# Optimization experiments

Measured on AMD Instinct MI355X. Metric: run time of the kernel, lower is better.

Reference implementation:

```python
import jax, jax.numpy as jnp
import numpy as np

GRID = 8
SPACING = 2.0
RADIUS = 3.0
B = 64
CODE = 1024
HID = 128
L = 4
EPS = 1e-5


def _layernorm(h, g, b):
    mu = h.mean(-1, keepdims=True)
    var = ((h - mu) ** 2).mean(-1, keepdims=True)
    return (h - mu) * jax.lax.rsqrt(var + EPS) * g + b


def setup_inputs() -> dict:
    key = jax.random.key(0)
    ks = jax.random.split(key, 16)
    n = GRID ** 3
    # grid coords, centered, spacing=anchor_spacing (create_grid_coords)
    idx = np.arange(GRID)
    coords = (np.stack(np.meshgrid(idx, idx, idx, indexing='ij'), -1).reshape(-1, 3)
              - (GRID - 1) / 2.0) * SPACING
    # radius_graph per batch: identical geometry per graph -> offset base edges
    d2 = ((coords[:, None, :] - coords[None, :, :]) ** 2).sum(-1)
    mask = (d2 <= RADIUS ** 2) & (d2 > 0)
    r0, c0 = np.nonzero(mask)
    off = (np.arange(B) * n)[:, None]
    row = (r0[None, :] + off).reshape(-1)
    col = (c0[None, :] + off).reshape(-1)
    edge_index = jnp.asarray(np.stack([row, col]), dtype=jnp.int32)  # [2,E]
    grid_coords = jnp.asarray(np.tile(coords, (B, 1)), dtype=jnp.float32)  # [B*n,3]
    s = 0.02
    inp = {
        'y': jax.random.normal(ks[0], (B, n, CODE), jnp.float32),
        'grid_coords': grid_coords,
        'edge_index': edge_index,
        'W_in': jax.random.normal(ks[1], (HID, CODE), jnp.float32) * s,
        'b_in': jnp.zeros((HID,), jnp.float32),
        'gam': jnp.ones((L, HID), jnp.float32),
        'bet': jnp.zeros((L, HID), jnp.float32),
        'eW1': jax.random.normal(ks[2], (L, HID, 2 * HID + 1), jnp.float32) * s,
        'eb1': jnp.zeros((L, HID), jnp.float32),
        'eW2': jax.random.normal(ks[3], (L, HID, HID), jnp.float32) * s,
        'eb2': jnp.zeros((L, HID), jnp.float32),
        'nW1': jax.random.normal(ks[4], (L, HID, 2 * HID), jnp.float32) * s,
        'nb1': jnp.zeros((L, HID), jnp.float32),
        'nW2': jax.random.normal(ks[5], (L, HID, HID), jnp.float32) * s,
        'nb2': jnp.zeros((L, HID), jnp.float32),
        'W_out': jax.random.normal(ks[6], (CODE, HID), jnp.float32) * s,
        'b_out': jnp.zeros((CODE,), jnp.float32),
    }
    return inp


def reference(y, grid_coords, edge_index, W_in, b_in, gam, bet,
              eW1, eb1, eW2, eb2, nW1, nb1, nW2, nb2, W_out, b_out):
    N = grid_coords.shape[0]  # B*n nodes
    row, col = edge_index[0], edge_index[1]
    rel = grid_coords[col] - grid_coords[row]            # [E,3]
    dist = jnp.linalg.norm(rel, axis=-1, keepdims=True)  # [E,1]
    cnt = jax.ops.segment_sum(jnp.ones((row.shape[0],), y.dtype), col, num_segments=N)
    inv_cnt = jnp.where(cnt > 0, 1.0 / jnp.maximum(cnt, 1.0), 0.0)[:, None]  # [N,1]

    h = jnp.einsum('bnc,hc->bnh', y, W_in) + b_in
    h = h.reshape(N, HID)
    for l in range(L):
        hn = _layernorm(h, gam[l], bet[l])               # [N,H]
        e_in = jnp.concatenate([hn[row], hn[col], dist], axis=-1)  # [E,2H+1]
        m = jax.nn.silu(e_in @ eW1[l].T + eb1[l])
        m = jax.nn.silu(m @ eW2[l].T + eb2[l])           # [E,H]
        m_aggr = jax.ops.segment_sum(m, col, num_segments=N) * inv_cnt  # scatter-mean
        d = jax.nn.silu(jnp.concatenate([hn, m_aggr], axis=-1) @ nW1[l].T + nb1[l])
        d = d @ nW2[l].T + nb2[l]
        h = hn + d                                        # residual on normalized h
    h = h.reshape(B, -1, HID)
    return jnp.einsum('bnh,ch->bnc', h, W_out) + b_out
```

## Files before the change

kernel.cpp:

```cpp
#include <hip/hip_runtime.h>
#include <math.h>


#define HIDDEN 128
#define NLAYERS 4
#define NBASE 512
#define NB 64
#define CODE 1024

typedef __attribute__((ext_vector_type(8))) short s16x8;
typedef __attribute__((ext_vector_type(4))) float f32x4;

__device__ __forceinline__ unsigned int cvt_pk_bf16(float lo, float hi) {
    unsigned int d;
    asm("v_cvt_pk_bf16_f32 %0, %1, %2" : "=v"(d) : "v"(lo), "v"(hi));
    return d;
}
__device__ __forceinline__ unsigned short f2bf(float x) {
    return (unsigned short)cvt_pk_bf16(x, x);
}
__device__ __forceinline__ float bf2f(unsigned short b) {
    return __uint_as_float(((unsigned int)b) << 16);
}
__device__ __forceinline__ float silu_f(float x) {
    float e = __expf(-x);
    float r;
    asm("v_rcp_f32 %0, %1" : "=v"(r) : "v"(1.f + e));
    return x * r;
}
__device__ __forceinline__ void light_barrier() {
    __builtin_amdgcn_sched_barrier(0);
    asm volatile("s_waitcnt lgkmcnt(0)" ::: "memory");
    __builtin_amdgcn_s_barrier();
    __builtin_amdgcn_sched_barrier(0);
}

__device__ __forceinline__ void conv_body(
    const float* __restrict__ s, unsigned short* __restrict__ d,
    int blk, int tid, int n) {
    int i = (blk * 256 + tid) * 4;
    if (i >= n) return;
    float4 v = *reinterpret_cast<const float4*>(s + i);
    uint2 o = { cvt_pk_bf16(v.x, v.y), cvt_pk_bf16(v.z, v.w) };
    *reinterpret_cast<uint2*>(d + i) = o;
}

__global__ __launch_bounds__(256) void prep_all(
    const float* __restrict__ W_in, const float* __restrict__ W_out,
    const float* __restrict__ nW1, const float* __restrict__ nW2,
    const float* __restrict__ eW2, const float* __restrict__ eW1,
    const float* __restrict__ eb1,
    const int* __restrict__ row, const int* __restrict__ col,
    const float* __restrict__ gc,
    unsigned short* __restrict__ winbf, unsigned short* __restrict__ woutbf,
    unsigned short* __restrict__ wn1bf, unsigned short* __restrict__ wn2bf,
    unsigned short* __restrict__ w2bf, unsigned short* __restrict__ w1ab,
    float* __restrict__ c01,
    int* __restrict__ brp, int* __restrict__ bcol, int baseE) {
    int blk = blockIdx.x, tid = threadIdx.x;
    if (blk < 128)      { conv_body(W_in,  winbf,  blk,       tid, HIDDEN * CODE); return; }
    if (blk < 256)      { conv_body(W_out, woutbf, blk - 128, tid, CODE * HIDDEN); return; }
    if (blk < 384)      { conv_body(nW1,   wn1bf,  blk - 256, tid, NLAYERS * HIDDEN * 256); return; }
    if (blk < 448)      { conv_body(nW2,   wn2bf,  blk - 384, tid, NLAYERS * HIDDEN * HIDDEN); return; }
    if (blk < 512)      { conv_body(eW2,   w2bf,   blk - 448, tid, NLAYERS * HIDDEN * HIDDEN); return; }
    if (blk < 516) {
        int l = blk - 512;
        const float* w = eW1 + (size_t)l * HIDDEN * 257;
        for (int i = tid; i < 256 * 128; i += 256) {
            int n = i >> 7, k = i & 127;
            float v = (n < 128) ? w[(size_t)n * 257 + k]
                                : w[(size_t)(n - 128) * 257 + 128 + k];
            w1ab[(size_t)l * 256 * 128 + i] = f2bf(v);
        }
        if (tid < 128) {
            float wd = w[(size_t)tid * 257 + 256];
            c01[(size_t)l * 256 + tid] = 2.f * wd;
            c01[(size_t)l * 256 + 128 + tid] = sqrtf(8.f) * wd;
        }
        return;
    }
    if (blk < 519) {
        int v = (blk - 516) * 256 + tid;
        if (v > NBASE) return;
        int lo = 0, hi = baseE;
        while (lo < hi) {
            int mid = (lo + hi) >> 1;
            if (row[mid] < v) lo = mid + 1; else hi = mid;
        }
        brp[v] = lo;
        return;
    }
    {
        int t = (blk - 519) * 256 + tid;
        if (t >= baseE) return;
        int u = col[t], v = row[t];
        float dx = gc[(size_t)u * 3 + 0] - gc[(size_t)v * 3 + 0];
        float dy = gc[(size_t)u * 3 + 1] - gc[(size_t)v * 3 + 1];
        float dz = gc[(size_t)u * 3 + 2] - gc[(size_t)v * 3 + 2];
        float d2 = dx * dx + dy * dy + dz * dz;
        bcol[t] = u | ((d2 > 6.f ? 1 : 0) << 15);
    }
}

__global__ __launch_bounds__(256) void mgemm64(
    const unsigned short* __restrict__ A, int K,
    const unsigned short* __restrict__ W,
    const float* __restrict__ bias,
    float* __restrict__ Cf, unsigned short* __restrict__ Cb, int ldC, int perm) {
    __shared__ __align__(16) unsigned short As[64 * 128];
    __shared__ __align__(16) unsigned short Ws[128 * 128];
    int tid = threadIdx.x;
    int wid = tid >> 6, l = tid & 63, lr = l & 15, lg = l >> 4;
    int wm = wid >> 1, wn = wid & 1;
    int row0 = blockIdx.x * 64;
    int cb = blockIdx.y * 128;
    f32x4 acc[2][4];
#pragma unroll
    for (int i = 0; i < 2; ++i)
#pragma unroll
        for (int j = 0; j < 4; ++j) {
            f32x4 z = { 0.f, 0.f, 0.f, 0.f };
            acc[i][j] = z;
        }
    for (int kc = 0; kc < K; kc += 128) {
#pragma unroll
        for (int jj = 0; jj < 4; ++jj) {
            int j = tid + jj * 256;
            int r = j >> 4, c = j & 15;
            int srow = row0 + r;
            if (perm == 3) srow = ((srow & 511) << 6) | (srow >> 9);
            s16x8 v = *reinterpret_cast<const s16x8*>(
                A + (size_t)srow * K + kc + c * 8);
            *reinterpret_cast<s16x8*>(&As[r * 128 + ((c ^ (r & 7)) << 3)]) = v;
        }
#pragma unroll
        for (int jj = 0; jj < 8; ++jj) {
            int j = tid + jj * 256;
            int r = j >> 4, c = j & 15;
            s16x8 wv = *reinterpret_cast<const s16x8*>(
                W + (size_t)(cb + r) * K + kc + c * 8);
            *reinterpret_cast<s16x8*>(&Ws[r * 128 + ((c ^ (r & 7)) << 3)]) = wv;
        }
        light_barrier();
#pragma unroll
        for (int ks = 0; ks < 4; ++ks) {
            int c = ks * 4 + lg;
            s16x8 af[2], bf[4];
#pragma unroll
            for (int mi = 0; mi < 2; ++mi) {
                int r = wm * 32 + mi * 16 + lr;
                af[mi] = *reinterpret_cast<s16x8*>(&As[r * 128 + ((c ^ (r & 7)) << 3)]);
            }
#pragma unroll
            for (int ni = 0; ni < 4; ++ni) {
                int n = wn * 64 + ni * 16 + lr;
                bf[ni] = *reinterpret_cast<s16x8*>(&Ws[n * 128 + ((c ^ (n & 7)) << 3)]);
            }
#pragma unroll
            for (int mi = 0; mi < 2; ++mi)
#pragma unroll
                for (int ni = 0; ni < 4; ++ni)
                    acc[mi][ni] = __builtin_amdgcn_mfma_f32_16x16x32_bf16(
                        af[mi], bf[ni], acc[mi][ni], 0, 0, 0);
        }
        light_barrier();
    }
#pragma unroll
    for (int mi = 0; mi < 2; ++mi) {
#pragma unroll
        for (int ni = 0; ni < 4; ++ni) {
            int colg = cb + wn * 64 + ni * 16 + lr;
            float bs = bias ? bias[colg] : 0.f;
#pragma unroll
            for (int r4 = 0; r4 < 4; ++r4) {
                int rowg = row0 + wm * 32 + mi * 16 + lg * 4 + r4;
                float v = acc[mi][ni][r4] + bs;
                if (Cf) Cf[(size_t)rowg * ldC + colg] = v;
                if (Cb) Cb[(size_t)rowg * ldC + colg] = f2bf(v);
            }
        }
    }
}

__global__ __launch_bounds__(256) void inproj_ln(
    const float* __restrict__ y,
    const unsigned short* __restrict__ W, const float* __restrict__ bias,
    const float* __restrict__ g, const float* __restrict__ bet,
    unsigned short* __restrict__ hnbf,
    const unsigned short* __restrict__ w1ab0,
    const float* __restrict__ eb1_0,
    unsigned short* __restrict__ ab_out) {
    __shared__ __align__(16) unsigned short As[64 * 128];
    __shared__ __align__(16) unsigned short Ws[128 * 128];
    int tid = threadIdx.x;
    int wid = tid >> 6, l = tid & 63, lr = l & 15, lg = l >> 4;
    int row0 = blockIdx.x * 64;
    f32x4 acc[8];
#pragma unroll
    for (int ni = 0; ni < 8; ++ni) {
        f32x4 z = { 0.f, 0.f, 0.f, 0.f };
        acc[ni] = z;
    }
    float4 pa0[4], pa1[4];
    s16x8 pw[8];
    auto loadc = [&](int kc) {
#pragma unroll
        for (int jj = 0; jj < 4; ++jj) {
            int j = tid + jj * 256, r = j >> 4, c = j & 15;
            const float* p = y + (size_t)(row0 + r) * CODE + kc + c * 8;
            pa0[jj] = *reinterpret_cast<const float4*>(p);
            pa1[jj] = *reinterpret_cast<const float4*>(p + 4);
        }
#pragma unroll
        for (int jj = 0; jj < 8; ++jj) {
            int j = tid + jj * 256, r = j >> 4, c = j & 15;
            pw[jj] = *reinterpret_cast<const s16x8*>(W + (size_t)r * CODE + kc + c * 8);
        }
    };
    auto storec = [&]() {
#pragma unroll
        for (int jj = 0; jj < 4; ++jj) {
            int j = tid + jj * 256, r = j >> 4, c = j & 15;
            union { s16x8 s; unsigned int w[4]; } pk;
            pk.w[0] = cvt_pk_bf16(pa0[jj].x, pa0[jj].y);
            pk.w[1] = cvt_pk_bf16(pa0[jj].z, pa0[jj].w);
            pk.w[2] = cvt_pk_bf16(pa1[jj].x, pa1[jj].y);
            pk.w[3] = cvt_pk_bf16(pa1[jj].z, pa1[jj].w);
            *reinterpret_cast<s16x8*>(&As[r * 128 + ((c ^ (r & 7)) << 3)]) = pk.s;
        }
#pragma unroll
        for (int jj = 0; jj < 8; ++jj) {
            int j = tid + jj * 256, r = j >> 4, c = j & 15;
            *reinterpret_cast<s16x8*>(&Ws[r * 128 + ((c ^ (r & 7)) << 3)]) = pw[jj];
        }
    };
    loadc(0);
    for (int kc8 = 0; kc8 < 8; ++kc8) {
        storec();
        light_barrier();
        if (kc8 < 7) loadc((kc8 + 1) * 128);
#pragma unroll
        for (int ks = 0; ks < 4; ++ks) {
            int c = ks * 4 + lg;
            int r = wid * 16 + lr;
            s16x8 af = *reinterpret_cast<s16x8*>(&As[r * 128 + ((c ^ (r & 7)) << 3)]);
#pragma unroll
            for (int ni = 0; ni < 8; ++ni) {
                int n = ni * 16 + lr;
                s16x8 bf = *reinterpret_cast<s16x8*>(&Ws[n * 128 + ((c ^ (n & 7)) << 3)]);
                acc[ni] = __builtin_amdgcn_mfma_f32_16x16x32_bf16(af, bf, acc[ni], 0, 0, 0);
            }
        }
        light_barrier();
    }
#pragma unroll
    for (int ni = 0; ni < 8; ++ni) {
        float bs = bias[ni * 16 + lr];
#pragma unroll
        for (int r4 = 0; r4 < 4; ++r4) acc[ni][r4] += bs;
    }
    float s[4], q[4];
#pragma unroll
    for (int r4 = 0; r4 < 4; ++r4) {
        float ss = 0.f, qq = 0.f;
#pragma unroll
        for (int ni = 0; ni < 8; ++ni) {
            float v = acc[ni][r4];
            ss += v; qq += v * v;
        }
#pragma unroll
        for (int o = 1; o < 16; o <<= 1) {
            ss += __shfl_xor(ss, o, 64);
            qq += __shfl_xor(qq, o, 64);
        }
        float mu = ss * (1.f / 128.f);
        float var = qq * (1.f / 128.f) - mu * mu;
        s[r4] = mu;
        q[r4] = rsqrtf(var + 1e-5f);
    }
#pragma unroll
    for (int ni = 0; ni < 8; ++ni) {
        int col = ni * 16 + lr;
        float gg = g[col], bb = bet[col];
        int cc = col >> 3, cin = col & 7;
#pragma unroll
        for (int r4 = 0; r4 < 4; ++r4) {
            int rowg = row0 + wid * 16 + lg * 4 + r4;
            int orow = (rowg & 511) * 64 + (rowg >> 9);
            float o = (acc[ni][r4] - s[r4]) * q[r4] * gg + bb;
            hnbf[(size_t)orow * HIDDEN + col] = f2bf(o);
            int rl = wid * 16 + lg * 4 + r4;
            As[rl * 128 + ((cc ^ (rl & 7)) << 3) + cin] = f2bf(o);
        }
    }
#pragma unroll
    for (int half = 0; half < 2; ++half) {
#pragma unroll
        for (int jj = 0; jj < 8; ++jj) {
            int j = tid + jj * 256;
            int r = j >> 4, c = j & 15;
            s16x8 wv = *reinterpret_cast<const s16x8*>(
                w1ab0 + (size_t)(half * 128 + r) * 128 + c * 8);
            *reinterpret_cast<s16x8*>(&Ws[r * 128 + ((c ^ (r & 7)) << 3)]) = wv;
        }
        light_barrier();
#pragma unroll
        for (int ni = 0; ni < 8; ++ni) {
            f32x4 z = { 0.f, 0.f, 0.f, 0.f };
            acc[ni] = z;
        }
#pragma unroll
        for (int ks = 0; ks < 4; ++ks) {
            int c = ks * 4 + lg;
            int r = wid * 16 + lr;
            s16x8 af = *reinterpret_cast<s16x8*>(&As[r * 128 + ((c ^ (r & 7)) << 3)]);
#pragma unroll
            for (int ni = 0; ni < 8; ++ni) {
                int n = ni * 16 + lr;
                s16x8 bf = *reinterpret_cast<s16x8*>(&Ws[n * 128 + ((c ^ (n & 7)) << 3)]);
                acc[ni] = __builtin_amdgcn_mfma_f32_16x16x32_bf16(af, bf, acc[ni], 0, 0, 0);
            }
        }
#pragma unroll
        for (int ni = 0; ni < 8; ++ni) {
            int col = ni * 16 + lr;
            float bs = half ? eb1_0[col] : 0.f;
#pragma unroll
            for (int r4 = 0; r4 < 4; ++r4) {
                int rowg = row0 + wid * 16 + lg * 4 + r4;
                int orow = (rowg & 511) * 64 + (rowg >> 9);
                ab_out[(size_t)orow * 256 + half * 128 + col] =
                    f2bf(acc[ni][r4] + bs);
            }
        }
        if (half == 0) light_barrier();
    }
}

__global__ __launch_bounds__(256) void nmlp_ln(
    unsigned short* __restrict__ hnbf,
    const unsigned short* __restrict__ magbf,
    const unsigned short* __restrict__ w1, const float* __restrict__ b1,
    const unsigned short* __restrict__ w2, const float* __restrict__ b2,
    const float* __restrict__ g, const float* __restrict__ bet,
    unsigned short* __restrict__ hbf_out,
    const unsigned short* __restrict__ w1ab_next,
    const float* __restrict__ eb1_next,
    unsigned short* __restrict__ ab_out) {
    __shared__ __align__(16) unsigned short As[64 * 128];
    __shared__ __align__(16) unsigned short Ws[128 * 128];
    int tid = threadIdx.x;
    int wid = tid >> 6, l = tid & 63, lr = l & 15, lg = l >> 4;
    int row0 = blockIdx.x * 64;
    int myrow = row0 + wid * 16 + lr;
    f32x4 acc[8];
#pragma unroll
    for (int ni = 0; ni < 8; ++ni) {
        f32x4 z = { 0.f, 0.f, 0.f, 0.f };
        acc[ni] = z;
    }
    for (int kc = 0; kc < 2; ++kc) {
        const unsigned short* Xsrc = kc ? magbf : hnbf;
#pragma unroll
        for (int jj = 0; jj < 8; ++jj) {
            int j = tid + jj * 256;
            int r = j >> 4, c = j & 15;
            s16x8 wv = *reinterpret_cast<const s16x8*>(
                w1 + (size_t)r * 256 + kc * 128 + c * 8);
            *reinterpret_cast<s16x8*>(&Ws[r * 128 + ((c ^ (r & 7)) << 3)]) = wv;
        }
        light_barrier();
#pragma unroll
        for (int ks = 0; ks < 4; ++ks) {
            s16x8 af = *reinterpret_cast<const s16x8*>(
                Xsrc + (size_t)myrow * 128 + ks * 32 + lg * 8);
#pragma unroll
            for (int ni = 0; ni < 8; ++ni) {
                int n = ni * 16 + lr;
                int c = ks * 4 + lg;
                s16x8 bf = *reinterpret_cast<s16x8*>(&Ws[n * 128 + ((c ^ (n & 7)) << 3)]);
                acc[ni] = __builtin_amdgcn_mfma_f32_16x16x32_bf16(af, bf, acc[ni], 0, 0, 0);
            }
        }
        light_barrier();
    }
#pragma unroll
    for (int ni = 0; ni < 8; ++ni) {
        int col = ni * 16 + lr;
        float bs = b1[col];
        int cc = col >> 3, cin = col & 7;
#pragma unroll
        for (int r4 = 0; r4 < 4; ++r4) {
            int rl = wid * 16 + lg * 4 + r4;
            As[rl * 128 + ((cc ^ (rl & 7)) << 3) + cin] =
                f2bf(silu_f(acc[ni][r4] + bs));
            acc[ni][r4] = 0.f;
        }
    }
#pragma unroll
    for (int jj = 0; jj < 8; ++jj) {
        int j = tid + jj * 256;
        int r = j >> 4, c = j & 15;
        s16x8 wv = *reinterpret_cast<const s16x8*>(w2 + (size_t)r * 128 + c * 8);
        *reinterpret_cast<s16x8*>(&Ws[r * 128 + ((c ^ (r & 7)) << 3)]) = wv;
    }
    light_barrier();
#pragma unroll
    for (int ks = 0; ks < 4; ++ks) {
        int c = ks * 4 + lg;
        int r = wid * 16 + lr;
        s16x8 af = *reinterpret_cast<s16x8*>(&As[r * 128 + ((c ^ (r & 7)) << 3)]);
#pragma unroll
        for (int ni = 0; ni < 8; ++ni) {
            int n = ni * 16 + lr;
            s16x8 bf = *reinterpret_cast<s16x8*>(&Ws[n * 128 + ((c ^ (n & 7)) << 3)]);
            acc[ni] = __builtin_amdgcn_mfma_f32_16x16x32_bf16(af, bf, acc[ni], 0, 0, 0);
        }
    }
#pragma unroll
    for (int ni = 0; ni < 8; ++ni) {
        int col = ni * 16 + lr;
        float bs = b2[col];
#pragma unroll
        for (int r4 = 0; r4 < 4; ++r4) {
            int rowg = row0 + wid * 16 + lg * 4 + r4;
            acc[ni][r4] += bs + bf2f(hnbf[(size_t)rowg * HIDDEN + col]);
        }
    }
    if (!g) {
#pragma unroll
        for (int ni = 0; ni < 8; ++ni) {
            int col = ni * 16 + lr;
#pragma unroll
            for (int r4 = 0; r4 < 4; ++r4) {
                int rowg = row0 + wid * 16 + lg * 4 + r4;
                hbf_out[(size_t)rowg * HIDDEN + col] = f2bf(acc[ni][r4]);
            }
        }
        return;
    }
    float s[4], q[4];
#pragma unroll
    for (int r4 = 0; r4 < 4; ++r4) {
        float ss = 0.f, qq = 0.f;
#pragma unroll
        for (int ni = 0; ni < 8; ++ni) {
            float v = acc[ni][r4];
            ss += v; qq += v * v;
        }
#pragma unroll
        for (int o = 1; o < 16; o <<= 1) {
            ss += __shfl_xor(ss, o, 64);
            qq += __shfl_xor(qq, o, 64);
        }
        float mu = ss * (1.f / 128.f);
        float var = qq * (1.f / 128.f) - mu * mu;
        s[r4] = mu;
        q[r4] = rsqrtf(var + 1e-5f);
    }
#pragma unroll
    for (int ni = 0; ni < 8; ++ni) {
        int col = ni * 16 + lr;
        float gg = g[col], bb = bet[col];
        int cc = col >> 3, cin = col & 7;
#pragma unroll
        for (int r4 = 0; r4 < 4; ++r4) {
            int rowg = row0 + wid * 16 + lg * 4 + r4;
            float o = (acc[ni][r4] - s[r4]) * q[r4] * gg + bb;
            hnbf[(size_t)rowg * HIDDEN + col] = f2bf(o);
            int rl = wid * 16 + lg * 4 + r4;
            As[rl * 128 + ((cc ^ (rl & 7)) << 3) + cin] = f2bf(o);
        }
    }
    light_barrier();
#pragma unroll
    for (int half = 0; half < 2; ++half) {
#pragma unroll
        for (int jj = 0; jj < 8; ++jj) {
            int j = tid + jj * 256;
            int r = j >> 4, c = j & 15;
            s16x8 wv = *reinterpret_cast<const s16x8*>(
                w1ab_next + (size_t)(half * 128 + r) * 128 + c * 8);
            *reinterpret_cast<s16x8*>(&Ws[r * 128 + ((c ^ (r & 7)) << 3)]) = wv;
        }
        light_barrier();
#pragma unroll
        for (int ni = 0; ni < 8; ++ni) {
            f32x4 z = { 0.f, 0.f, 0.f, 0.f };
            acc[ni] = z;
        }
#pragma unroll
        for (int ks = 0; ks < 4; ++ks) {
            int c = ks * 4 + lg;
            int r = wid * 16 + lr;
            s16x8 af = *reinterpret_cast<s16x8*>(&As[r * 128 + ((c ^ (r & 7)) << 3)]);
#pragma unroll
            for (int ni = 0; ni < 8; ++ni) {
                int n = ni * 16 + lr;
                s16x8 bf = *reinterpret_cast<s16x8*>(&Ws[n * 128 + ((c ^ (n & 7)) << 3)]);
                acc[ni] = __builtin_amdgcn_mfma_f32_16x16x32_bf16(af, bf, acc[ni], 0, 0, 0);
            }
        }
#pragma unroll
        for (int ni = 0; ni < 8; ++ni) {
            int col = ni * 16 + lr;
            float bs = half ? eb1_next[col] : 0.f;
#pragma unroll
            for (int r4 = 0; r4 < 4; ++r4) {
                int rowg = row0 + wid * 16 + lg * 4 + r4;
                ab_out[(size_t)rowg * 256 + half * 128 + col] =
                    f2bf(acc[ni][r4] + bs);
            }
        }
        if (half == 0) light_barrier();
    }
}

__global__ __launch_bounds__(256, 4) void edge_mfma9(
    const unsigned short* __restrict__ ABbf,
    const int* __restrict__ bcol,
    const int* __restrict__ brp,
    const unsigned short* __restrict__ w2bf,
    const float* __restrict__ c01,
    const float* __restrict__ eb2l,
    unsigned short* __restrict__ magbf) {
    __shared__ __align__(16) unsigned short m1[8][16 * 128];
    int tid = threadIdx.x;
    int blk = blockIdx.x;
    int i = blk >> 2, qtr = blk & 3;
    int wid = tid >> 6, l = tid & 63, lr = l & 15, lg = l >> 4;
    int rowb = qtr * 16;
    int col0 = wid * 32;

    s16x8 wfr[4][2];
#pragma unroll
    for (int ks = 0; ks < 4; ++ks)
#pragma unroll
        for (int ni = 0; ni < 2; ++ni) {
            int n = col0 + ni * 16 + lr;
            wfr[ks][ni] = *reinterpret_cast<const s16x8*>(
                w2bf + (size_t)n * 128 + (ks * 4 + lg) * 8);
        }

    int s = brp[i], e = brp[i + 1];
    int br = tid >> 4, bc = tid & 15;
    s16x8 Bp[2];
    {
        union { s16x8 s; unsigned int w[4]; } bv;
        bv.s = *reinterpret_cast<const s16x8*>(
            ABbf + ((size_t)i * NB + rowb + br) * 256 + 128 + bc * 8);
#pragma unroll
        for (int cls = 0; cls < 2; ++cls) {
            const float* cp = c01 + cls * 128 + bc * 8;
            float4 ca = *reinterpret_cast<const float4*>(cp);
            float4 cb = *reinterpret_cast<const float4*>(cp + 4);
            union { s16x8 s; unsigned int w[4]; } pk;
            pk.w[0] = cvt_pk_bf16(__uint_as_float(bv.w[0] << 16) + ca.x,
                                  __uint_as_float(bv.w[0] & 0xffff0000u) + ca.y);
            pk.w[1] = cvt_pk_bf16(__uint_as_float(bv.w[1] << 16) + ca.z,
                                  __uint_as_float(bv.w[1] & 0xffff0000u) + ca.w);
            pk.w[2] = cvt_pk_bf16(__uint_as_float(bv.w[2] << 16) + cb.x,
                                  __uint_as_float(bv.w[2] & 0xffff0000u) + cb.y);
            pk.w[3] = cvt_pk_bf16(__uint_as_float(bv.w[3] << 16) + cb.z,
                                  __uint_as_float(bv.w[3] & 0xffff0000u) + cb.w);
            Bp[cls] = pk.s;
        }
    }
    float e2[2], se[2];
#pragma unroll
    for (int ni = 0; ni < 2; ++ni) {
        e2[ni] = eb2l[col0 + ni * 16 + lr];
        se[ni] = silu_f(e2[ni]);
    }
    f32x4 agg[2];
#pragma unroll
    for (int ni = 0; ni < 2; ++ni) {
        f32x4 z = { 0.f, 0.f, 0.f, 0.f };
        agg[ni] = z;
    }

    auto loadA = [&](int t, int& pk) -> s16x8 {
        pk = __builtin_amdgcn_readfirstlane(bcol[t]);
        return *reinterpret_cast<const s16x8*>(
            ABbf + ((size_t)(pk & 0x7fff) * NB + rowb + br) * 256 + bc * 8);
    };
    auto build = [&](s16x8 A, int cls, int buf) {
        union { s16x8 s; unsigned int w[4]; } av, bv2, pkv;
        av.s = A;
        bv2.s = cls ? Bp[1] : Bp[0];
#pragma unroll
        for (int q = 0; q < 4; ++q) {
            float a0 = __uint_as_float(av.w[q] << 16);
            float a1 = __uint_as_float(av.w[q] & 0xffff0000u);
            float b0 = __uint_as_float(bv2.w[q] << 16);
            float b1 = __uint_as_float(bv2.w[q] & 0xffff0000u);
            pkv.w[q] = cvt_pk_bf16(silu_f(a0 + b0), silu_f(a1 + b1));
        }
        *reinterpret_cast<s16x8*>(
            &m1[buf][br * 128 + ((bc ^ (br & 7)) << 3)]) = pkv.s;
    };
    auto mfma_epi = [&](int buf) {
        f32x4 acc[2];
#pragma unroll
        for (int ni = 0; ni < 2; ++ni) {
            f32x4 iv = { e2[ni], e2[ni], e2[ni], e2[ni] };
            acc[ni] = iv;
        }
#pragma unroll
        for (int ks = 0; ks < 4; ++ks) {
            int cc = ks * 4 + lg;
            s16x8 af = *reinterpret_cast<s16x8*>(
                &m1[buf][lr * 128 + ((cc ^ (lr & 7)) << 3)]);
            acc[0] = __builtin_amdgcn_mfma_f32_16x16x32_bf16(af, wfr[ks][0], acc[0], 0, 0, 0);
            acc[1] = __builtin_amdgcn_mfma_f32_16x16x32_bf16(af, wfr[ks][1], acc[1], 0, 0, 0);
        }
#pragma unroll
        for (int ni = 0; ni < 2; ++ni)
#pragma unroll
            for (int r4 = 0; r4 < 4; ++r4)
                agg[ni][r4] += silu_f(acc[ni][r4]) - se[ni];
    };

    int pk[4];
    s16x8 A[4];
    A[0] = loadA(s, pk[0]);
#pragma unroll
    for (int k = 1; k < 4; ++k) {
        pk[k] = pk[0];
        A[k] = A[0];
    }
#pragma unroll
    for (int k = 1; k < 4; ++k)
        if (s + k < e) A[k] = loadA(s + k, pk[k]);

    for (int t = s; t < e; t += 4) {
        int qb = (((t - s) >> 2) & 1) << 2;
        int pkn[4];
        s16x8 An[4];
#pragma unroll
        for (int k = 0; k < 4; ++k) {
            pkn[k] = pk[k];
            An[k] = A[k];
        }
#pragma unroll
        for (int k = 0; k < 4; ++k)
            if (t + 4 + k < e) An[k] = loadA(t + 4 + k, pkn[k]);
        build(A[0], (pk[0] >> 15) & 1, qb);
#pragma unroll
        for (int k = 1; k < 4; ++k)
            if (t + k < e) build(A[k], (pk[k] >> 15) & 1, qb + k);
        light_barrier();
        mfma_epi(qb);
#pragma unroll
        for (int k = 1; k < 4; ++k)
            if (t + k < e) mfma_epi(qb + k);
#pragma unroll
        for (int k = 0; k < 4; ++k) {
            pk[k] = pkn[k];
            A[k] = An[k];
        }
    }

    float inv = (e > s) ? 1.f / (float)(e - s) : 0.f;
#pragma unroll
    for (int ni = 0; ni < 2; ++ni) {
#pragma unroll
        for (int r4 = 0; r4 < 4; ++r4) {
            size_t rowg = (size_t)i * NB + rowb + lg * 4 + r4;
            magbf[rowg * 128 + col0 + ni * 16 + lr] =
                f2bf(agg[ni][r4] * inv + se[ni]);
        }
    }
}

extern "C" void kernel_launch(void* const* d_in, const int* in_sizes, int n_in,
                              void* d_out, int out_size, void* d_ws, size_t ws_size,
                              hipStream_t stream) {
    const float* y     = (const float*)d_in[0];
    const float* gc    = (const float*)d_in[1];
    const int*   eidx  = (const int*)d_in[2];
    const float* W_in  = (const float*)d_in[3];
    const float* b_in  = (const float*)d_in[4];
    const float* gam   = (const float*)d_in[5];
    const float* bet   = (const float*)d_in[6];
    const float* eW1   = (const float*)d_in[7];
    const float* eb1   = (const float*)d_in[8];
    const float* eW2   = (const float*)d_in[9];
    const float* eb2   = (const float*)d_in[10];
    const float* nW1   = (const float*)d_in[11];
    const float* nb1   = (const float*)d_in[12];
    const float* nW2   = (const float*)d_in[13];
    const float* nb2   = (const float*)d_in[14];
    const float* W_out = (const float*)d_in[15];
    const float* b_out = (const float*)d_in[16];

    const int M = in_sizes[0] / CODE;
    const int E = in_sizes[2] / 2;
    const int baseE = E / NB;

    float* out = (float*)d_out;

    char* ws = (char*)d_ws;
    size_t off = 0;
    auto carve = [&](size_t bytes) {
        char* p = ws + off;
        off += (bytes + 255) & ~(size_t)255;
        return p;
    };
    unsigned short* hnbf    = (unsigned short*)carve((size_t)M * HIDDEN * 2);
    unsigned short* ABbf    = (unsigned short*)carve((size_t)M * 256 * 2);
    unsigned short* magbf   = (unsigned short*)carve((size_t)M * HIDDEN * 2);
    unsigned short* hbf     = (unsigned short*)carve((size_t)M * HIDDEN * 2);
    int*            brp     = (int*)carve((size_t)(NBASE + 1) * 4);
    int*            bcol    = (int*)carve((size_t)baseE * 4);
    unsigned short* winbf   = (unsigned short*)carve((size_t)HIDDEN * CODE * 2);
    unsigned short* woutbf  = (unsigned short*)carve((size_t)CODE * HIDDEN * 2);
    unsigned short* wn1bf   = (unsigned short*)carve((size_t)NLAYERS * HIDDEN * 256 * 2);
    unsigned short* wn2bf   = (unsigned short*)carve((size_t)NLAYERS * HIDDEN * HIDDEN * 2);
    unsigned short* w2bf    = (unsigned short*)carve((size_t)NLAYERS * HIDDEN * HIDDEN * 2);
    unsigned short* w1ab    = (unsigned short*)carve((size_t)NLAYERS * 256 * HIDDEN * 2);
    float*          c01     = (float*)carve((size_t)NLAYERS * 256 * 4);

    const int* row  = eidx;
    const int* colA = eidx + E;

    int prep_blocks = 519 + (baseE + 255) / 256;
    prep_all<<<dim3(prep_blocks), 256, 0, stream>>>(
        W_in, W_out, nW1, nW2, eW2, eW1, eb1, row, colA, gc,
        winbf, woutbf, wn1bf, wn2bf, w2bf, w1ab, c01,
        brp, bcol, baseE);

    inproj_ln<<<dim3(M / 64), 256, 0, stream>>>(
        y, winbf, b_in, gam, bet, hnbf, w1ab, eb1, ABbf);

    for (int l = 0; l < NLAYERS; ++l) {
        edge_mfma9<<<dim3(NBASE * 4), 256, 0, stream>>>(
            ABbf, bcol, brp,
            w2bf + (size_t)l * HIDDEN * HIDDEN, c01 + (size_t)l * 256,
            eb2 + (size_t)l * HIDDEN, magbf);

        bool last = (l == NLAYERS - 1);
        nmlp_ln<<<dim3(M / 64), 256, 0, stream>>>(
            hnbf, magbf,
            wn1bf + (size_t)l * HIDDEN * 256, nb1 + (size_t)l * HIDDEN,
            wn2bf + (size_t)l * HIDDEN * HIDDEN, nb2 + (size_t)l * HIDDEN,
            last ? nullptr : gam + (size_t)(l + 1) * HIDDEN,
            last ? nullptr : bet + (size_t)(l + 1) * HIDDEN,
            hbf,
            last ? nullptr : w1ab + (size_t)(l + 1) * 256 * HIDDEN,
            last ? nullptr : eb1 + (size_t)(l + 1) * HIDDEN,
            last ? nullptr : ABbf);
    }

    mgemm64<<<dim3(M / 64, CODE / 128), 256, 0, stream>>>(
        hbf, HIDDEN, woutbf, b_out, out, nullptr, CODE, 3);
}
```

Baseline: 399.9 us.

## Split edge kernel work by edge per wave with shared W2 in LDS

The edge kernel now gives each wave its own edges, one full 16x128 tile per edge, instead of splitting output columns across waves. W2 is staged once into swizzled LDS, and the first-layer activations are built straight into MFMA A-fragment registers, so the per-iteration LDS staging and barriers go away. Partial aggregates from the four waves are reduced through LDS at the end. The cost is more registers (launch bounds drop to 3 blocks), 32 KB of LDS per block, and possible load imbalance when an edge count is not a multiple of four.

```diff
diff --git a/kernel.cpp b/kernel.cpp
--- a/kernel.cpp
+++ b/kernel.cpp
@@ -516,7 +516,7 @@
     }
 }
 
-__global__ __launch_bounds__(256, 4) void edge_mfma9(
+__global__ __launch_bounds__(256, 3) void edge_mfma10(
     const unsigned short* __restrict__ ABbf,
     const int* __restrict__ bcol,
     const int* __restrict__ brp,
@@ -524,151 +524,171 @@
     const float* __restrict__ c01,
     const float* __restrict__ eb2l,
     unsigned short* __restrict__ magbf) {
-    __shared__ __align__(16) unsigned short m1[8][16 * 128];
+    __shared__ __align__(16) unsigned short w2s[128 * 128];
     int tid = threadIdx.x;
     int blk = blockIdx.x;
     int i = blk >> 2, qtr = blk & 3;
     int wid = tid >> 6, l = tid & 63, lr = l & 15, lg = l >> 4;
     int rowb = qtr * 16;
-    int col0 = wid * 32;
-
-    s16x8 wfr[4][2];
-#pragma unroll
-    for (int ks = 0; ks < 4; ++ks)
-#pragma unroll
-        for (int ni = 0; ni < 2; ++ni) {
-            int n = col0 + ni * 16 + lr;
-            wfr[ks][ni] = *reinterpret_cast<const s16x8*>(
-                w2bf + (size_t)n * 128 + (ks * 4 + lg) * 8);
-        }
+
+    for (int jj = tid; jj < 2048; jj += 256) {
+        int n = jj >> 4, c = jj & 15;
+        s16x8 w = *reinterpret_cast<const s16x8*>(w2bf + (size_t)n * 128 + c * 8);
+        *reinterpret_cast<s16x8*>(&w2s[n * 128 + ((c ^ (n & 7)) << 3)]) = w;
+    }
 
     int s = brp[i], e = brp[i + 1];
-    int br = tid >> 4, bc = tid & 15;
-    s16x8 Bp[2];
+
+    s16x8 Bp0[4], Bp1[4];
     {
-        union { s16x8 s; unsigned int w[4]; } bv;
-        bv.s = *reinterpret_cast<const s16x8*>(
-            ABbf + ((size_t)i * NB + rowb + br) * 256 + 128 + bc * 8);
-#pragma unroll
-        for (int cls = 0; cls < 2; ++cls) {
-            const float* cp = c01 + cls * 128 + bc * 8;
-            float4 ca = *reinterpret_cast<const float4*>(cp);
-            float4 cb = *reinterpret_cast<const float4*>(cp + 4);
-            union { s16x8 s; unsigned int w[4]; } pk;
-            pk.w[0] = cvt_pk_bf16(__uint_as_float(bv.w[0] << 16) + ca.x,
-                                  __uint_as_float(bv.w[0] & 0xffff0000u) + ca.y);
-            pk.w[1] = cvt_pk_bf16(__uint_as_float(bv.w[1] << 16) + ca.z,
-                                  __uint_as_float(bv.w[1] & 0xffff0000u) + ca.w);
-            pk.w[2] = cvt_pk_bf16(__uint_as_float(bv.w[2] << 16) + cb.x,
-                                  __uint_as_float(bv.w[2] & 0xffff0000u) + cb.y);
-            pk.w[3] = cvt_pk_bf16(__uint_as_float(bv.w[3] << 16) + cb.z,
-                                  __uint_as_float(bv.w[3] & 0xffff0000u) + cb.w);
-            Bp[cls] = pk.s;
-        }
-    }
-    float e2[2], se[2];
-#pragma unroll
-    for (int ni = 0; ni < 2; ++ni) {
-        e2[ni] = eb2l[col0 + ni * 16 + lr];
-        se[ni] = silu_f(e2[ni]);
-    }
-    f32x4 agg[2];
-#pragma unroll
-    for (int ni = 0; ni < 2; ++ni) {
+        const unsigned short* Brow = ABbf + ((size_t)i * NB + rowb + lr) * 256 + 128;
+#pragma unroll
+        for (int ks = 0; ks < 4; ++ks) {
+            int ch = ks * 32 + lg * 8;
+            union { s16x8 s; unsigned int w[4]; } bv;
+            bv.s = *reinterpret_cast<const s16x8*>(Brow + ch);
+            const float* cp0 = c01 + ch;
+            const float* cp1 = c01 + 128 + ch;
+            float4 a0 = *reinterpret_cast<const float4*>(cp0);
+            float4 a1 = *reinterpret_cast<const float4*>(cp0 + 4);
+            float4 b0 = *reinterpret_cast<const float4*>(cp1);
+            float4 b1 = *reinterpret_cast<const float4*>(cp1 + 4);
+            union { s16x8 s; unsigned int w[4]; } p0, p1;
+            p0.w[0] = cvt_pk_bf16(__uint_as_float(bv.w[0] << 16) + a0.x,
+                                  __uint_as_float(bv.w[0] & 0xffff0000u) + a0.y);
+            p0.w[1] = cvt_pk_bf16(__uint_as_float(bv.w[1] << 16) + a0.z,
+                                  __uint_as_float(bv.w[1] & 0xffff0000u) + a0.w);
+            p0.w[2] = cvt_pk_bf16(__uint_as_float(bv.w[2] << 16) + a1.x,
+                                  __uint_as_float(bv.w[2] & 0xffff0000u) + a1.y);
+            p0.w[3] = cvt_pk_bf16(__uint_as_float(bv.w[3] << 16) + a1.z,
+                                  __uint_as_float(bv.w[3] & 0xffff0000u) + a1.w);
+            p1.w[0] = cvt_pk_bf16(__uint_as_float(bv.w[0] << 16) + b0.x,
+                                  __uint_as_float(bv.w[0] & 0xffff0000u) + b0.y);
+            p1.w[1] = cvt_pk_bf16(__uint_as_float(bv.w[1] << 16) + b0.z,
+                                  __uint_as_float(bv.w[1] & 0xffff0000u) + b0.w);
+            p1.w[2] = cvt_pk_bf16(__uint_as_float(bv.w[2] << 16) + b1.x,
+                                  __uint_as_float(bv.w[2] & 0xffff0000u) + b1.y);
+            p1.w[3] = cvt_pk_bf16(__uint_as_float(bv.w[3] << 16) + b1.z,
+                                  __uint_as_float(bv.w[3] & 0xffff0000u) + b1.w);
+            Bp0[ks] = p0.s;
+            Bp1[ks] = p1.s;
+        }
+    }
+    float e2[8], se[8];
+#pragma unroll
+    for (int nf = 0; nf < 8; ++nf) {
+        e2[nf] = eb2l[nf * 16 + lr];
+        se[nf] = silu_f(e2[nf]);
+    }
+    f32x4 agg[8];
+#pragma unroll
+    for (int nf = 0; nf < 8; ++nf) {
         f32x4 z = { 0.f, 0.f, 0.f, 0.f };
-        agg[ni] = z;
-    }
-
-    auto loadA = [&](int t, int& pk) -> s16x8 {
-        pk = __builtin_amdgcn_readfirstlane(bcol[t]);
-        return *reinterpret_cast<const s16x8*>(
-            ABbf + ((size_t)(pk & 0x7fff) * NB + rowb + br) * 256 + bc * 8);
-    };
-    auto build = [&](s16x8 A, int cls, int buf) {
-        union { s16x8 s; unsigned int w[4]; } av, bv2, pkv;
-        av.s = A;
-        bv2.s = cls ? Bp[1] : Bp[0];
-#pragma unroll
-        for (int q = 0; q < 4; ++q) {
-            float a0 = __uint_as_float(av.w[q] << 16);
-            float a1 = __uint_as_float(av.w[q] & 0xffff0000u);
-            float b0 = __uint_as_float(bv2.w[q] << 16);
-            float b1 = __uint_as_float(bv2.w[q] & 0xffff0000u);
-            pkv.w[q] = cvt_pk_bf16(silu_f(a0 + b0), silu_f(a1 + b1));
-        }
-        *reinterpret_cast<s16x8*>(
-            &m1[buf][br * 128 + ((bc ^ (br & 7)) << 3)]) = pkv.s;
-    };
-    auto mfma_epi = [&](int buf) {
-        f32x4 acc[2];
-#pragma unroll
-        for (int ni = 0; ni < 2; ++ni) {
-            f32x4 iv = { e2[ni], e2[ni], e2[ni], e2[ni] };
-            acc[ni] = iv;
-        }
+        agg[nf] = z;
+    }
+    light_barrier();
+
+    int t = s + wid;
+    int pk0 = 0;
+    s16x8 A[4];
+    if (t < e) {
+        pk0 = __builtin_amdgcn_readfirstlane(bcol[t]);
+        const unsigned short* Ar =
+            ABbf + ((size_t)(pk0 & 0x7fff) * NB + rowb + lr) * 256;
+#pragma unroll
+        for (int ks = 0; ks < 4; ++ks)
+            A[ks] = *reinterpret_cast<const s16x8*>(Ar + ks * 32 + lg * 8);
+    }
+    while (t < e) {
+        int tn = t + 4;
+        int pkn = pk0;
+        s16x8 An[4];
+#pragma unroll
+        for (int ks = 0; ks < 4; ++ks) An[ks] = A[ks];
+        if (tn < e) {
+            pkn = __builtin_amdgcn_readfirstlane(bcol[tn]);
+            const unsigned short* Ar =
+                ABbf + ((size_t)(pkn & 0x7fff) * NB + rowb + lr) * 256;
+#pragma unroll
+            for (int ks = 0; ks < 4; ++ks)
+                An[ks] = *reinterpret_cast<const s16x8*>(Ar + ks * 32 + lg * 8);
+        }
+        int cls = (pk0 >> 15) & 1;
+        s16x8 af[4];
 #pragma unroll
         for (int ks = 0; ks < 4; ++ks) {
-            int cc = ks * 4 + lg;
-            s16x8 af = *reinterpret_cast<s16x8*>(
-                &m1[buf][lr * 128 + ((cc ^ (lr & 7)) << 3)]);
-            acc[0] = __builtin_amdgcn_mfma_f32_16x16x32_bf16(af, wfr[ks][0], acc[0], 0, 0, 0);
-            acc[1] = __builtin_amdgcn_mfma_f32_16x16x32_bf16(af, wfr[ks][1], acc[1], 0, 0, 0);
-        }
-#pragma unroll
-        for (int ni = 0; ni < 2; ++ni)
+            union { s16x8 s; unsigned int w[4]; } av, bv, pkv;
+            av.s = A[ks];
+            bv.s = cls ? Bp1[ks] : Bp0[ks];
+#pragma unroll
+            for (int q = 0; q < 4; ++q) {
+                float a0 = __uint_as_float(av.w[q] << 16);
+                float a1 = __uint_as_float(av.w[q] & 0xffff0000u);
+                float b0 = __uint_as_float(bv.w[q] << 16);
+                float b1 = __uint_as_float(bv.w[q] & 0xffff0000u);
+                pkv.w[q] = cvt_pk_bf16(silu_f(a0 + b0), silu_f(a1 + b1));
+            }
+            af[ks] = pkv.s;
+        }
+#pragma unroll
+        for (int half = 0; half < 2; ++half) {
+            f32x4 acc[4];
+#pragma unroll
+            for (int n4 = 0; n4 < 4; ++n4) {
+                int nf = half * 4 + n4;
+                f32x4 iv = { e2[nf], e2[nf], e2[nf], e2[nf] };
+                acc[n4] = iv;
+            }
+#pragma unroll
+            for (int ks = 0; ks < 4; ++ks) {
+                int cc = ks * 4 + lg;
+#pragma unroll
+                for (int n4 = 0; n4 < 4; ++n4) {
+                    int n = (half * 4 + n4) * 16 + lr;
+                    s16x8 bf = *reinterpret_cast<s16x8*>(
+                        &w2s[n * 128 + ((cc ^ (n & 7)) << 3)]);
+                    acc[n4] = __builtin_amdgcn_mfma_f32_16x16x32_bf16(
+                        af[ks], bf, acc[n4], 0, 0, 0);
+                }
+            }
+#pragma unroll
+            for (int n4 = 0; n4 < 4; ++n4) {
+                int nf = half * 4 + n4;
+#pragma unroll
+                for (int r4 = 0; r4 < 4; ++r4)
+                    agg[nf][r4] += silu_f(acc[n4][r4]) - se[nf];
+            }
+        }
+        t = tn;
+        pk0 = pkn;
+#pragma unroll
+        for (int ks = 0; ks < 4; ++ks) A[ks] = An[ks];
+    }
+
+    light_barrier();
+    float* cmb = reinterpret_cast<float*>(w2s);
+    if (wid != 0) {
+#pragma unroll
+        for (int nf = 0; nf < 8; ++nf)
 #pragma unroll
             for (int r4 = 0; r4 < 4; ++r4)
-                agg[ni][r4] += silu_f(acc[ni][r4]) - se[ni];
-    };
-
-    int pk[4];
-    s16x8 A[4];
-    A[0] = loadA(s, pk[0]);
-#pragma unroll
-    for (int k = 1; k < 4; ++k) {
-        pk[k] = pk[0];
-        A[k] = A[0];
-    }
-#pragma unroll
-    for (int k = 1; k < 4; ++k)
-        if (s + k < e) A[k] = loadA(s + k, pk[k]);
-
-    for (int t = s; t < e; t += 4) {
-        int qb = (((t - s) >> 2) & 1) << 2;
-        int pkn[4];
-        s16x8 An[4];
-#pragma unroll
-        for (int k = 0; k < 4; ++k) {
-            pkn[k] = pk[k];
-            An[k] = A[k];
-        }
-#pragma unroll
-        for (int k = 0; k < 4; ++k)
-            if (t + 4 + k < e) An[k] = loadA(t + 4 + k, pkn[k]);
-        build(A[0], (pk[0] >> 15) & 1, qb);
-#pragma unroll
-        for (int k = 1; k < 4; ++k)
-            if (t + k < e) build(A[k], (pk[k] >> 15) & 1, qb + k);
-        light_barrier();
-        mfma_epi(qb);
-#pragma unroll
-        for (int k = 1; k < 4; ++k)
-            if (t + k < e) mfma_epi(qb + k);
-#pragma unroll
-        for (int k = 0; k < 4; ++k) {
-            pk[k] = pkn[k];
-            A[k] = An[k];
-        }
-    }
-
-    float inv = (e > s) ? 1.f / (float)(e - s) : 0.f;
-#pragma unroll
-    for (int ni = 0; ni < 2; ++ni) {
-#pragma unroll
-        for (int r4 = 0; r4 < 4; ++r4) {
-            size_t rowg = (size_t)i * NB + rowb + lg * 4 + r4;
-            magbf[rowg * 128 + col0 + ni * 16 + lr] =
-                f2bf(agg[ni][r4] * inv + se[ni]);
+                cmb[(wid - 1) * 2112 + (lg * 4 + r4) * 132 + nf * 16 + lr] =
+                    agg[nf][r4];
+    }
+    light_barrier();
+    if (wid == 0) {
+        float inv = (e > s) ? 1.f / (float)(e - s) : 0.f;
+#pragma unroll
+        for (int nf = 0; nf < 8; ++nf) {
+#pragma unroll
+            for (int r4 = 0; r4 < 4; ++r4) {
+                float tot = agg[nf][r4];
+#pragma unroll
+                for (int w = 0; w < 3; ++w)
+                    tot += cmb[w * 2112 + (lg * 4 + r4) * 132 + nf * 16 + lr];
+                size_t rowg = (size_t)i * NB + rowb + lg * 4 + r4;
+                magbf[rowg * 128 + nf * 16 + lr] = f2bf(tot * inv + se[nf]);
+            }
         }
     }
 }
@@ -734,7 +754,7 @@
         y, winbf, b_in, gam, bet, hnbf, w1ab, eb1, ABbf);
 
     for (int l = 0; l < NLAYERS; ++l) {
-        edge_mfma9<<<dim3(NBASE * 4), 256, 0, stream>>>(
+        edge_mfma10<<<dim3(NBASE * 4), 256, 0, stream>>>(
             ABbf, bcol, brp,
             w2bf + (size_t)l * HIDDEN * HIDDEN, c01 + (size_t)l * 256,
             eb2 + (size_t)l * HIDDEN, magbf);
```

Result: slower. 542.0 us (+35.5%).
